# Kernel tuning notes

Hardware: AMD Instinct MI355X
Metric: run time of the kernel (lower is better)

Reference implementation:

```python
import jax, jax.numpy as jnp
import numpy as np

EPS = 1e-3


def setup_inputs() -> dict:
    key = jax.random.key(0)
    kq, kk, kv, kp = jax.random.split(key, 4)
    B, H, L, d = 4, 8, 8192, 64
    num_rows = int(d * np.log(d))  # 266, as in PerformerProjection
    q = jax.random.normal(kq, (B, H, L, d), dtype=jnp.float32)
    k = jax.random.normal(kk, (B, H, L, d), dtype=jnp.float32)
    v = jax.random.normal(kv, (B, H, L, d), dtype=jnp.float32)
    # Orthogonal-block projection matrix [num_rows, d] via QR (matches buffer init)
    rng = np.random.default_rng(0)
    blocks = []
    rows_left = num_rows
    while rows_left > 0:
        m = rng.standard_normal((d, d)).astype(np.float32)
        qm, _ = np.linalg.qr(m)
        blocks.append(qm.T[: min(d, rows_left)])
        rows_left -= d
    proj = jnp.asarray(np.concatenate(blocks, axis=0))  # [num_rows, d]
    return {"q": q, "k": k, "v": v, "proj": proj}


def reference(q, k, v, proj):
    # generalized_kernel: x @ proj.T, ReLU, + eps  -> features [B,H,L,R]
    qp = jax.nn.relu(jnp.einsum("bhld,rd->bhlr", q, proj)) + EPS
    kp = jax.nn.relu(jnp.einsum("bhld,rd->bhlr", k, proj)) + EPS
    # linear attention: D^{-1} (Q' ((K')^T V))
    k_sum = kp.sum(axis=-2)                       # [B,H,R]
    d_inv = 1.0 / jnp.einsum("bhlr,bhr->bhl", qp, k_sum)  # [B,H,L]
    kv = jnp.einsum("bhlr,bhld->bhrd", kp, v)     # [B,H,R,d]
    out = jnp.einsum("bhlr,bhrd->bhld", qp, kv)   # [B,H,L,d]
    return out * d_inv[..., None]
```

## Files before the change

### kernel.cpp

```cpp
#include <hip/hip_runtime.h>

typedef __attribute__((ext_vector_type(8))) short short8;
typedef __attribute__((ext_vector_type(4))) float f32x4;

#define MFMA16(a,b,c) __builtin_amdgcn_mfma_f32_16x16x32_bf16((a),(b),(c),0,0,0)

constexpr int BHC = 32;
constexpr int LEN = 8192;
constexpr int DD  = 64;
constexpr int RR  = 266;
constexpr int RP  = 272;
constexpr float EPSF = 1e-3f;

__device__ __forceinline__ unsigned short f2bf(float x) {
  unsigned u = __builtin_bit_cast(unsigned, x);
  return (unsigned short)((u + 0x7FFFu + ((u >> 16) & 1u)) >> 16);
}
__device__ __forceinline__ float bf2f(unsigned short h) {
  return __builtin_bit_cast(float, (unsigned)h << 16);
}
__device__ __forceinline__ void split2(float x, unsigned short& h, unsigned short& l) {
  h = f2bf(x);
  l = f2bf(x - bf2f(h));
}

__global__ __launch_bounds__(512, 1) void perf_kv_kernel(
    const float* __restrict__ kin, const float* __restrict__ vin,
    const float* __restrict__ proj,
    float* __restrict__ kv_ws, float* __restrict__ ksum_ws)
{
  __shared__ unsigned short K_hi[32*72], K_lo[32*72];
  __shared__ float V_lds[32*68];
  __shared__ unsigned int fT_hi[RP*20], fT_lo[RP*20];

  const int t = threadIdx.x;
  const int wid = t >> 6, lane = t & 63, g = lane >> 4, ln = lane & 15;
  const int bh = blockIdx.y;
  const float* kb = kin + (size_t)bh * LEN * DD + (size_t)blockIdx.x * 1024 * DD;
  const float* vb = vin + (size_t)bh * LEN * DD + (size_t)blockIdx.x * 1024 * DD;

  const int nrt1 = (wid == 7) ? 3 : 2;
  short8 Ph[3][2], Pl[3][2];
#pragma unroll
  for (int j = 0; j < 3; ++j) {
    const int rt = (j == 2) ? 16 : 2 * wid + j;
#pragma unroll
    for (int c = 0; c < 2; ++c) {
      const int r = rt * 16 + ln;
      float pv[8];
      if (j < nrt1 && r < RR) {
        const float4 a = *(const float4*)&proj[r * DD + c * 32 + g * 8];
        const float4 b = *(const float4*)&proj[r * DD + c * 32 + g * 8 + 4];
        pv[0]=a.x; pv[1]=a.y; pv[2]=a.z; pv[3]=a.w;
        pv[4]=b.x; pv[5]=b.y; pv[6]=b.z; pv[7]=b.w;
      } else {
#pragma unroll
        for (int i = 0; i < 8; ++i) pv[i] = 0.f;
      }
#pragma unroll
      for (int i = 0; i < 8; ++i) {
        unsigned short h, l; split2(pv[i], h, l);
        Ph[j][c][i] = (short)h; Pl[j][c][i] = (short)l;
      }
    }
  }

  f32x4 kvacc[9];
#pragma unroll
  for (int j = 0; j < 9; ++j) kvacc[j] = (f32x4){0.f,0.f,0.f,0.f};
  float ksacc[3] = {0.f, 0.f, 0.f};

  const int dt = wid & 3;
  const int rbase2 = (wid >> 2) * 9;
  const int nrt2 = (wid >> 2) ? 8 : 9;

  for (int s = 0; s < 32; ++s) {
    {
      const int l = t >> 4, c4 = t & 15;
      const float4 kv4 = *(const float4*)&kb[(size_t)(s*32 + l) * DD + c4*4];
      const float4 vv4 = *(const float4*)&vb[(size_t)(s*32 + l) * DD + c4*4];
      unsigned short h0,q0,h1,q1,h2,q2,h3,q3;
      split2(kv4.x,h0,q0); split2(kv4.y,h1,q1); split2(kv4.z,h2,q2); split2(kv4.w,h3,q3);
      *(ushort4*)&K_hi[l*72 + c4*4] = make_ushort4(h0,h1,h2,h3);
      *(ushort4*)&K_lo[l*72 + c4*4] = make_ushort4(q0,q1,q2,q3);
      *(float4*)&V_lds[l*68 + c4*4] = vv4;
    }
    __syncthreads();

    short8 KAh[2][2], KAl[2][2];
#pragma unroll
    for (int lt = 0; lt < 2; ++lt)
#pragma unroll
    for (int c = 0; c < 2; ++c) {
      KAh[lt][c] = *(const short8*)&K_hi[(lt*16+ln)*72 + c*32 + g*8];
      KAl[lt][c] = *(const short8*)&K_lo[(lt*16+ln)*72 + c*32 + g*8];
    }
#pragma unroll
    for (int j = 0; j < 3; ++j) if (j < nrt1) {
      const int rt = (j == 2) ? 16 : 2*wid + j;
      const int r = rt*16 + ln;
      const bool rok = r < RR;
#pragma unroll
      for (int lt = 0; lt < 2; ++lt) {
        f32x4 acc = {0.f,0.f,0.f,0.f};
#pragma unroll
        for (int c = 0; c < 2; ++c) {
          acc = MFMA16(KAh[lt][c], Ph[j][c], acc);
          acc = MFMA16(KAh[lt][c], Pl[j][c], acc);
          acc = MFMA16(KAl[lt][c], Ph[j][c], acc);
        }
        unsigned short h[4], q[4];
        float sum = 0.f;
#pragma unroll
        for (int reg = 0; reg < 4; ++reg) {
          const float fv = rok ? (fmaxf(acc[reg], 0.f) + EPSF) : 0.f;
          sum += fv;
          split2(fv, h[reg], q[reg]);
        }
        ksacc[j] += sum;
        *(uint2*)&fT_hi[r*20 + lt*8 + g*2] =
            make_uint2((unsigned)h[0] | ((unsigned)h[1]<<16),
                       (unsigned)h[2] | ((unsigned)h[3]<<16));
        *(uint2*)&fT_lo[r*20 + lt*8 + g*2] =
            make_uint2((unsigned)q[0] | ((unsigned)q[1]<<16),
                       (unsigned)q[2] | ((unsigned)q[3]<<16));
      }
    }
    __syncthreads();

    short8 VAh, VAl;
#pragma unroll
    for (int i = 0; i < 8; ++i) {
      const float v = V_lds[(g*8 + i)*68 + dt*16 + ln];
      unsigned short h, l; split2(v, h, l);
      VAh[i] = (short)h; VAl[i] = (short)l;
    }
#pragma unroll
    for (int j = 0; j < 9; ++j) if (j < nrt2) {
      const int rt = rbase2 + j;
      const short8 Bh = *(const short8*)&fT_hi[(rt*16+ln)*20 + g*4];
      const short8 Bl = *(const short8*)&fT_lo[(rt*16+ln)*20 + g*4];
      f32x4 a = kvacc[j];
      a = MFMA16(VAh, Bh, a);
      a = MFMA16(VAh, Bl, a);
      a = MFMA16(VAl, Bh, a);
      kvacc[j] = a;
    }
    __syncthreads();
  }

  float* kvb = kv_ws + (size_t)bh * DD * RP;
#pragma unroll
  for (int j = 0; j < 9; ++j) if (j < nrt2) {
    const int rt = rbase2 + j;
#pragma unroll
    for (int reg = 0; reg < 4; ++reg)
      atomicAdd(&kvb[(dt*16 + g*4 + reg) * RP + rt*16 + ln], kvacc[j][reg]);
  }
#pragma unroll
  for (int j = 0; j < 3; ++j) if (j < nrt1) {
    const int rt = (j == 2) ? 16 : 2*wid + j;
    float v = ksacc[j];
    v += __shfl_xor(v, 16);
    v += __shfl_xor(v, 32);
    if (lane < 16) atomicAdd(&ksum_ws[bh * RP + rt*16 + lane], v);
  }
}

__global__ __launch_bounds__(512, 1) void perf_out_kernel(
    const float* __restrict__ qin, const float* __restrict__ proj,
    const float* __restrict__ kv_ws, const float* __restrict__ ksum_ws,
    float* __restrict__ out)
{
  __shared__ unsigned short P_hi[RP*72], P_lo[RP*72];
  __shared__ unsigned short feat_hi[32*296], feat_lo[32*296];
  __shared__ unsigned short Q_hi[32*72], Q_lo[32*72];
  __shared__ float ksum_lds[RP];
  __shared__ float den_l[32];

  const int t = threadIdx.x;
  const int wid = t >> 6, lane = t & 63, g = lane >> 4, ln = lane & 15;
  const int bh = blockIdx.y;
  const float* qb = qin + (size_t)bh * LEN * DD + (size_t)blockIdx.x * 1024 * DD;
  float* ob = out + (size_t)bh * LEN * DD + (size_t)blockIdx.x * 1024 * DD;

  for (int idx = t; idx < RP * 16; idx += 512) {
    const int row = idx >> 4, c4 = idx & 15;
    float4 val = make_float4(0.f, 0.f, 0.f, 0.f);
    if (row < RR) val = *(const float4*)&proj[row * DD + c4 * 4];
    unsigned short h0,q0,h1,q1,h2,q2,h3,q3;
    split2(val.x,h0,q0); split2(val.y,h1,q1); split2(val.z,h2,q2); split2(val.w,h3,q3);
    *(ushort4*)&P_hi[row*72 + c4*4] = make_ushort4(h0,h1,h2,h3);
    *(ushort4*)&P_lo[row*72 + c4*4] = make_ushort4(q0,q1,q2,q3);
  }
  for (int idx = t; idx < 32 * 32; idx += 512) {
    const int row = idx >> 5, c = 272 + (idx & 31);
    if (c < 296) { feat_hi[row*296 + c] = 0; feat_lo[row*296 + c] = 0; }
  }
  if (t < RP) ksum_lds[t] = ksum_ws[bh*RP + t];

  const int dt = wid & 3;
  short8 KVh[9], KVl[9];
  {
    const float* kvr = kv_ws + ((size_t)bh*DD + dt*16 + ln) * RP;
#pragma unroll
    for (int kc = 0; kc < 9; ++kc) {
      const int r0 = kc*32 + g*8;
      float pv[8];
      if (r0 + 7 < RP) {
        const float4 a = *(const float4*)&kvr[r0];
        const float4 b = *(const float4*)&kvr[r0 + 4];
        pv[0]=a.x; pv[1]=a.y; pv[2]=a.z; pv[3]=a.w;
        pv[4]=b.x; pv[5]=b.y; pv[6]=b.z; pv[7]=b.w;
      } else {
#pragma unroll
        for (int i = 0; i < 8; ++i) pv[i] = 0.f;
      }
#pragma unroll
      for (int i = 0; i < 8; ++i) {
        unsigned short h, l; split2(pv[i], h, l);
        KVh[kc][i] = (short)h; KVl[kc][i] = (short)l;
      }
    }
  }

  const int nrt1 = (wid >= 6) ? 3 : 2;
  const int lt4 = wid >> 2, dt4 = wid & 3;

  __syncthreads();

  for (int s = 0; s < 32; ++s) {
    {
      const int l = t >> 4, c4 = t & 15;
      const float4 qv4 = *(const float4*)&qb[(size_t)(s*32 + l) * DD + c4*4];
      unsigned short h0,q0,h1,q1,h2,q2,h3,q3;
      split2(qv4.x,h0,q0); split2(qv4.y,h1,q1); split2(qv4.z,h2,q2); split2(qv4.w,h3,q3);
      *(ushort4*)&Q_hi[l*72 + c4*4] = make_ushort4(h0,h1,h2,h3);
      *(ushort4*)&Q_lo[l*72 + c4*4] = make_ushort4(q0,q1,q2,q3);
      if (t < 32) den_l[t] = 0.f;
    }
    __syncthreads();

#pragma unroll
    for (int j = 0; j < 3; ++j) if (j < nrt1) {
      const int rt = (j == 2) ? 16 : 2*wid + j;
      short8 PAh[2], PAl[2];
#pragma unroll
      for (int c = 0; c < 2; ++c) {
        PAh[c] = *(const short8*)&P_hi[(rt*16+ln)*72 + c*32 + g*8];
        PAl[c] = *(const short8*)&P_lo[(rt*16+ln)*72 + c*32 + g*8];
      }
#pragma unroll
      for (int lt = 0; lt < 2; ++lt) {
        if (j == 2 && lt != (wid & 1)) continue;
        f32x4 acc = {0.f,0.f,0.f,0.f};
#pragma unroll
        for (int c = 0; c < 2; ++c) {
          const short8 QBh = *(const short8*)&Q_hi[(lt*16+ln)*72 + c*32 + g*8];
          const short8 QBl = *(const short8*)&Q_lo[(lt*16+ln)*72 + c*32 + g*8];
          acc = MFMA16(PAh[c], QBh, acc);
          acc = MFMA16(PAh[c], QBl, acc);
          acc = MFMA16(PAl[c], QBh, acc);
        }
        unsigned short h[4], q[4];
        float dacc = 0.f;
#pragma unroll
        for (int reg = 0; reg < 4; ++reg) {
          const int r = rt*16 + g*4 + reg;
          const float fv = (r < RR) ? (fmaxf(acc[reg], 0.f) + EPSF) : 0.f;
          dacc += fv * ksum_lds[r];
          split2(fv, h[reg], q[reg]);
        }
        atomicAdd(&den_l[lt*16 + ln], dacc);
        *(ushort4*)&feat_hi[(lt*16+ln)*296 + rt*16 + g*4] = make_ushort4(h[0],h[1],h[2],h[3]);
        *(ushort4*)&feat_lo[(lt*16+ln)*296 + rt*16 + g*4] = make_ushort4(q[0],q[1],q[2],q[3]);
      }
    }
    __syncthreads();

    f32x4 oacc = {0.f,0.f,0.f,0.f};
#pragma unroll
    for (int kc = 0; kc < 9; ++kc) {
      const short8 Ah = *(const short8*)&feat_hi[(lt4*16+ln)*296 + kc*32 + g*8];
      const short8 Al = *(const short8*)&feat_lo[(lt4*16+ln)*296 + kc*32 + g*8];
      oacc = MFMA16(Ah, KVh[kc], oacc);
      oacc = MFMA16(Ah, KVl[kc], oacc);
      oacc = MFMA16(Al, KVh[kc], oacc);
    }
#pragma unroll
    for (int reg = 0; reg < 4; ++reg) {
      const int l = lt4*16 + g*4 + reg;
      ob[(size_t)(s*32 + l) * DD + dt4*16 + ln] = oacc[reg] / den_l[l];
    }
    __syncthreads();
  }
}

extern "C" void kernel_launch(void* const* d_in, const int* in_sizes, int n_in,
                              void* d_out, int out_size, void* d_ws, size_t ws_size,
                              hipStream_t stream) {
  (void)in_sizes; (void)n_in; (void)out_size; (void)ws_size;
  const float* q    = (const float*)d_in[0];
  const float* k    = (const float*)d_in[1];
  const float* v    = (const float*)d_in[2];
  const float* proj = (const float*)d_in[3];
  float* out     = (float*)d_out;
  float* kv_ws   = (float*)d_ws;
  float* ksum_ws = kv_ws + (size_t)BHC * DD * RP;

  size_t zbytes = ((size_t)BHC * DD * RP + (size_t)BHC * RP) * sizeof(float);
  hipMemsetAsync(d_ws, 0, zbytes, stream);

  perf_kv_kernel<<<dim3(8, BHC), dim3(512), 0, stream>>>(k, v, proj, kv_ws, ksum_ws);
  perf_out_kernel<<<dim3(8, BHC), dim3(512), 0, stream>>>(q, proj, kv_ws, ksum_ws, out);
}
```

Before: 450.6 us.

## Double grid size, reload projection per tile, and trim barriers in both kernels

Both kernels now process 512 rows per block instead of 1024, doubling the grid to 16x32 blocks so more CUs are busy. Projection fragments are no longer held in registers or an LDS copy; they are reloaded from global memory (L1/L2-cached) per tile, which frees registers and LDS. V is read straight from global instead of being staged through LDS. The next K/Q tile is loaded after the mid-iteration barrier, removing one sync per iteration, and den_l is double-buffered. MFMA accumulation is split into three independent chains to shorten dependency latency, at the cost of extra proj loads and twice as many atomic flushes to the workspace.

```diff
diff --git a/kernel.cpp b/kernel.cpp
--- a/kernel.cpp
+++ b/kernel.cpp
@@ -30,113 +30,107 @@
     float* __restrict__ kv_ws, float* __restrict__ ksum_ws)
 {
   __shared__ unsigned short K_hi[32*72], K_lo[32*72];
-  __shared__ float V_lds[32*68];
   __shared__ unsigned int fT_hi[RP*20], fT_lo[RP*20];
 
   const int t = threadIdx.x;
   const int wid = t >> 6, lane = t & 63, g = lane >> 4, ln = lane & 15;
   const int bh = blockIdx.y;
-  const float* kb = kin + (size_t)bh * LEN * DD + (size_t)blockIdx.x * 1024 * DD;
-  const float* vb = vin + (size_t)bh * LEN * DD + (size_t)blockIdx.x * 1024 * DD;
+  const float* kb = kin + (size_t)bh*LEN*DD + (size_t)blockIdx.x*512*DD;
+  const float* vb = vin + (size_t)bh*LEN*DD + (size_t)blockIdx.x*512*DD;
 
   const int nrt1 = (wid == 7) ? 3 : 2;
-  short8 Ph[3][2], Pl[3][2];
-#pragma unroll
-  for (int j = 0; j < 3; ++j) {
-    const int rt = (j == 2) ? 16 : 2 * wid + j;
-#pragma unroll
-    for (int c = 0; c < 2; ++c) {
-      const int r = rt * 16 + ln;
-      float pv[8];
-      if (j < nrt1 && r < RR) {
-        const float4 a = *(const float4*)&proj[r * DD + c * 32 + g * 8];
-        const float4 b = *(const float4*)&proj[r * DD + c * 32 + g * 8 + 4];
-        pv[0]=a.x; pv[1]=a.y; pv[2]=a.z; pv[3]=a.w;
-        pv[4]=b.x; pv[5]=b.y; pv[6]=b.z; pv[7]=b.w;
-      } else {
-#pragma unroll
-        for (int i = 0; i < 8; ++i) pv[i] = 0.f;
-      }
-#pragma unroll
-      for (int i = 0; i < 8; ++i) {
-        unsigned short h, l; split2(pv[i], h, l);
-        Ph[j][c][i] = (short)h; Pl[j][c][i] = (short)l;
-      }
-    }
-  }
+  const int dt = wid & 3, rbase2 = (wid >> 2) * 9, nrt2 = (wid >> 2) ? 8 : 9;
 
   f32x4 kvacc[9];
 #pragma unroll
   for (int j = 0; j < 9; ++j) kvacc[j] = (f32x4){0.f,0.f,0.f,0.f};
-  float ksacc[3] = {0.f, 0.f, 0.f};
-
-  const int dt = wid & 3;
-  const int rbase2 = (wid >> 2) * 9;
-  const int nrt2 = (wid >> 2) ? 8 : 9;
-
-  for (int s = 0; s < 32; ++s) {
-    {
-      const int l = t >> 4, c4 = t & 15;
-      const float4 kv4 = *(const float4*)&kb[(size_t)(s*32 + l) * DD + c4*4];
-      const float4 vv4 = *(const float4*)&vb[(size_t)(s*32 + l) * DD + c4*4];
-      unsigned short h0,q0,h1,q1,h2,q2,h3,q3;
-      split2(kv4.x,h0,q0); split2(kv4.y,h1,q1); split2(kv4.z,h2,q2); split2(kv4.w,h3,q3);
-      *(ushort4*)&K_hi[l*72 + c4*4] = make_ushort4(h0,h1,h2,h3);
-      *(ushort4*)&K_lo[l*72 + c4*4] = make_ushort4(q0,q1,q2,q3);
-      *(float4*)&V_lds[l*68 + c4*4] = vv4;
-    }
-    __syncthreads();
-
-    short8 KAh[2][2], KAl[2][2];
-#pragma unroll
-    for (int lt = 0; lt < 2; ++lt)
-#pragma unroll
-    for (int c = 0; c < 2; ++c) {
-      KAh[lt][c] = *(const short8*)&K_hi[(lt*16+ln)*72 + c*32 + g*8];
-      KAl[lt][c] = *(const short8*)&K_lo[(lt*16+ln)*72 + c*32 + g*8];
-    }
-#pragma unroll
-    for (int j = 0; j < 3; ++j) if (j < nrt1) {
-      const int rt = (j == 2) ? 16 : 2*wid + j;
-      const int r = rt*16 + ln;
-      const bool rok = r < RR;
-#pragma unroll
-      for (int lt = 0; lt < 2; ++lt) {
-        f32x4 acc = {0.f,0.f,0.f,0.f};
+  float ksacc[3] = {0.f,0.f,0.f};
+
+  const int sl = t >> 4, sc = t & 15;
+  {
+    const float4 k4 = *(const float4*)&kb[(size_t)sl*DD + sc*4];
+    unsigned short h0,q0,h1,q1,h2,q2,h3,q3;
+    split2(k4.x,h0,q0); split2(k4.y,h1,q1); split2(k4.z,h2,q2); split2(k4.w,h3,q3);
+    *(ushort4*)&K_hi[sl*72 + sc*4] = make_ushort4(h0,h1,h2,h3);
+    *(ushort4*)&K_lo[sl*72 + sc*4] = make_ushort4(q0,q1,q2,q3);
+  }
+  __syncthreads();
+
+  for (int s = 0; s < 16; ++s) {
+#pragma unroll
+    for (int lt = 0; lt < 2; ++lt) {
+      short8 KAh[2], KAl[2];
+#pragma unroll
+      for (int c = 0; c < 2; ++c) {
+        KAh[c] = *(const short8*)&K_hi[(lt*16+ln)*72 + c*32 + g*8];
+        KAl[c] = *(const short8*)&K_lo[(lt*16+ln)*72 + c*32 + g*8];
+      }
+#pragma unroll
+      for (int j = 0; j < 3; ++j) {
+        if (j >= nrt1) break;
+        const int rt = (j == 2) ? 16 : 2*wid + j;
+        const int r = rt*16 + ln;
+        const bool rok = r < RR;
+        short8 PBh[2], PBl[2];
 #pragma unroll
         for (int c = 0; c < 2; ++c) {
-          acc = MFMA16(KAh[lt][c], Ph[j][c], acc);
-          acc = MFMA16(KAh[lt][c], Pl[j][c], acc);
-          acc = MFMA16(KAl[lt][c], Ph[j][c], acc);
+          float pv[8];
+          if (rok) {
+            const float4 a = *(const float4*)&proj[r*DD + c*32 + g*8];
+            const float4 b = *(const float4*)&proj[r*DD + c*32 + g*8 + 4];
+            pv[0]=a.x; pv[1]=a.y; pv[2]=a.z; pv[3]=a.w;
+            pv[4]=b.x; pv[5]=b.y; pv[6]=b.z; pv[7]=b.w;
+          } else {
+#pragma unroll
+            for (int i2 = 0; i2 < 8; ++i2) pv[i2] = 0.f;
+          }
+#pragma unroll
+          for (int i2 = 0; i2 < 8; ++i2) {
+            unsigned short h, l2; split2(pv[i2], h, l2);
+            PBh[c][i2] = (short)h; PBl[c][i2] = (short)l2;
+          }
+        }
+        f32x4 a0 = {0.f,0.f,0.f,0.f}, a1 = a0, a2 = a0;
+#pragma unroll
+        for (int c = 0; c < 2; ++c) {
+          a0 = MFMA16(KAh[c], PBh[c], a0);
+          a1 = MFMA16(KAh[c], PBl[c], a1);
+          a2 = MFMA16(KAl[c], PBh[c], a2);
         }
         unsigned short h[4], q[4];
         float sum = 0.f;
 #pragma unroll
         for (int reg = 0; reg < 4; ++reg) {
-          const float fv = rok ? (fmaxf(acc[reg], 0.f) + EPSF) : 0.f;
+          const float fv = rok ? (fmaxf(a0[reg]+a1[reg]+a2[reg], 0.f) + EPSF) : 0.f;
           sum += fv;
           split2(fv, h[reg], q[reg]);
         }
         ksacc[j] += sum;
         *(uint2*)&fT_hi[r*20 + lt*8 + g*2] =
-            make_uint2((unsigned)h[0] | ((unsigned)h[1]<<16),
-                       (unsigned)h[2] | ((unsigned)h[3]<<16));
+            make_uint2((unsigned)h[0]|((unsigned)h[1]<<16), (unsigned)h[2]|((unsigned)h[3]<<16));
         *(uint2*)&fT_lo[r*20 + lt*8 + g*2] =
-            make_uint2((unsigned)q[0] | ((unsigned)q[1]<<16),
-                       (unsigned)q[2] | ((unsigned)q[3]<<16));
+            make_uint2((unsigned)q[0]|((unsigned)q[1]<<16), (unsigned)q[2]|((unsigned)q[3]<<16));
       }
     }
     __syncthreads();
 
+    if (s < 15) {
+      const float4 k4 = *(const float4*)&kb[(size_t)((s+1)*32 + sl)*DD + sc*4];
+      unsigned short h0,q0,h1,q1,h2,q2,h3,q3;
+      split2(k4.x,h0,q0); split2(k4.y,h1,q1); split2(k4.z,h2,q2); split2(k4.w,h3,q3);
+      *(ushort4*)&K_hi[sl*72 + sc*4] = make_ushort4(h0,h1,h2,h3);
+      *(ushort4*)&K_lo[sl*72 + sc*4] = make_ushort4(q0,q1,q2,q3);
+    }
     short8 VAh, VAl;
 #pragma unroll
     for (int i = 0; i < 8; ++i) {
-      const float v = V_lds[(g*8 + i)*68 + dt*16 + ln];
-      unsigned short h, l; split2(v, h, l);
-      VAh[i] = (short)h; VAl[i] = (short)l;
-    }
-#pragma unroll
-    for (int j = 0; j < 9; ++j) if (j < nrt2) {
+      const float v = vb[(size_t)(s*32 + g*8 + i)*DD + dt*16 + ln];
+      unsigned short h, l2; split2(v, h, l2);
+      VAh[i] = (short)h; VAl[i] = (short)l2;
+    }
+#pragma unroll
+    for (int j = 0; j < 9; ++j) {
+      if (j >= nrt2) break;
       const int rt = rbase2 + j;
       const short8 Bh = *(const short8*)&fT_hi[(rt*16+ln)*20 + g*4];
       const short8 Bl = *(const short8*)&fT_lo[(rt*16+ln)*20 + g*4];
@@ -151,19 +145,21 @@
 
   float* kvb = kv_ws + (size_t)bh * DD * RP;
 #pragma unroll
-  for (int j = 0; j < 9; ++j) if (j < nrt2) {
+  for (int j = 0; j < 9; ++j) {
+    if (j >= nrt2) break;
     const int rt = rbase2 + j;
 #pragma unroll
     for (int reg = 0; reg < 4; ++reg)
-      atomicAdd(&kvb[(dt*16 + g*4 + reg) * RP + rt*16 + ln], kvacc[j][reg]);
-  }
-#pragma unroll
-  for (int j = 0; j < 3; ++j) if (j < nrt1) {
+      atomicAdd(&kvb[(dt*16 + g*4 + reg)*RP + rt*16 + ln], kvacc[j][reg]);
+  }
+#pragma unroll
+  for (int j = 0; j < 3; ++j) {
+    if (j >= nrt1) break;
     const int rt = (j == 2) ? 16 : 2*wid + j;
     float v = ksacc[j];
     v += __shfl_xor(v, 16);
     v += __shfl_xor(v, 32);
-    if (lane < 16) atomicAdd(&ksum_ws[bh * RP + rt*16 + lane], v);
+    if (lane < 16) atomicAdd(&ksum_ws[bh*RP + rt*16 + lane], v);
   }
 }
 
@@ -172,37 +168,37 @@
     const float* __restrict__ kv_ws, const float* __restrict__ ksum_ws,
     float* __restrict__ out)
 {
-  __shared__ unsigned short P_hi[RP*72], P_lo[RP*72];
+  __shared__ unsigned short Q_hi[32*72], Q_lo[32*72];
   __shared__ unsigned short feat_hi[32*296], feat_lo[32*296];
-  __shared__ unsigned short Q_hi[32*72], Q_lo[32*72];
   __shared__ float ksum_lds[RP];
-  __shared__ float den_l[32];
+  __shared__ float den_l[2][32];
 
   const int t = threadIdx.x;
   const int wid = t >> 6, lane = t & 63, g = lane >> 4, ln = lane & 15;
   const int bh = blockIdx.y;
-  const float* qb = qin + (size_t)bh * LEN * DD + (size_t)blockIdx.x * 1024 * DD;
-  float* ob = out + (size_t)bh * LEN * DD + (size_t)blockIdx.x * 1024 * DD;
-
-  for (int idx = t; idx < RP * 16; idx += 512) {
-    const int row = idx >> 4, c4 = idx & 15;
-    float4 val = make_float4(0.f, 0.f, 0.f, 0.f);
-    if (row < RR) val = *(const float4*)&proj[row * DD + c4 * 4];
+  const float* qb = qin + (size_t)bh*LEN*DD + (size_t)blockIdx.x*512*DD;
+  float* outb = out + (size_t)bh*LEN*DD + (size_t)blockIdx.x*512*DD;
+
+  for (int idx = t; idx < 32*24; idx += 512) {
+    const int row = idx / 24, c = 272 + idx % 24;
+    feat_hi[row*296 + c] = 0; feat_lo[row*296 + c] = 0;
+  }
+  if (t < RP) ksum_lds[t] = ksum_ws[bh*RP + t];
+  if (t < 32) den_l[0][t] = 0.f;
+
+  const int sl = t >> 4, sc = t & 15;
+  {
+    const float4 q4 = *(const float4*)&qb[(size_t)sl*DD + sc*4];
     unsigned short h0,q0,h1,q1,h2,q2,h3,q3;
-    split2(val.x,h0,q0); split2(val.y,h1,q1); split2(val.z,h2,q2); split2(val.w,h3,q3);
-    *(ushort4*)&P_hi[row*72 + c4*4] = make_ushort4(h0,h1,h2,h3);
-    *(ushort4*)&P_lo[row*72 + c4*4] = make_ushort4(q0,q1,q2,q3);
-  }
-  for (int idx = t; idx < 32 * 32; idx += 512) {
-    const int row = idx >> 5, c = 272 + (idx & 31);
-    if (c < 296) { feat_hi[row*296 + c] = 0; feat_lo[row*296 + c] = 0; }
-  }
-  if (t < RP) ksum_lds[t] = ksum_ws[bh*RP + t];
-
-  const int dt = wid & 3;
+    split2(q4.x,h0,q0); split2(q4.y,h1,q1); split2(q4.z,h2,q2); split2(q4.w,h3,q3);
+    *(ushort4*)&Q_hi[sl*72 + sc*4] = make_ushort4(h0,h1,h2,h3);
+    *(ushort4*)&Q_lo[sl*72 + sc*4] = make_ushort4(q0,q1,q2,q3);
+  }
+
+  const int lt4 = wid >> 2, dt4 = wid & 3;
   short8 KVh[9], KVl[9];
   {
-    const float* kvr = kv_ws + ((size_t)bh*DD + dt*16 + ln) * RP;
+    const float* kvr = kv_ws + ((size_t)bh*DD + dt4*16 + ln) * RP;
 #pragma unroll
     for (int kc = 0; kc < 9; ++kc) {
       const int r0 = kc*32 + g*8;
@@ -218,79 +214,95 @@
       }
 #pragma unroll
       for (int i = 0; i < 8; ++i) {
-        unsigned short h, l; split2(pv[i], h, l);
-        KVh[kc][i] = (short)h; KVl[kc][i] = (short)l;
+        unsigned short h, l2; split2(pv[i], h, l2);
+        KVh[kc][i] = (short)h; KVl[kc][i] = (short)l2;
       }
     }
   }
 
   const int nrt1 = (wid >= 6) ? 3 : 2;
-  const int lt4 = wid >> 2, dt4 = wid & 3;
-
   __syncthreads();
 
-  for (int s = 0; s < 32; ++s) {
-    {
-      const int l = t >> 4, c4 = t & 15;
-      const float4 qv4 = *(const float4*)&qb[(size_t)(s*32 + l) * DD + c4*4];
-      unsigned short h0,q0,h1,q1,h2,q2,h3,q3;
-      split2(qv4.x,h0,q0); split2(qv4.y,h1,q1); split2(qv4.z,h2,q2); split2(qv4.w,h3,q3);
-      *(ushort4*)&Q_hi[l*72 + c4*4] = make_ushort4(h0,h1,h2,h3);
-      *(ushort4*)&Q_lo[l*72 + c4*4] = make_ushort4(q0,q1,q2,q3);
-      if (t < 32) den_l[t] = 0.f;
-    }
-    __syncthreads();
-
-#pragma unroll
-    for (int j = 0; j < 3; ++j) if (j < nrt1) {
-      const int rt = (j == 2) ? 16 : 2*wid + j;
-      short8 PAh[2], PAl[2];
+  for (int s = 0; s < 16; ++s) {
+#pragma unroll
+    for (int lt = 0; lt < 2; ++lt) {
+      short8 QBh[2], QBl[2];
 #pragma unroll
       for (int c = 0; c < 2; ++c) {
-        PAh[c] = *(const short8*)&P_hi[(rt*16+ln)*72 + c*32 + g*8];
-        PAl[c] = *(const short8*)&P_lo[(rt*16+ln)*72 + c*32 + g*8];
-      }
-#pragma unroll
-      for (int lt = 0; lt < 2; ++lt) {
+        QBh[c] = *(const short8*)&Q_hi[(lt*16+ln)*72 + c*32 + g*8];
+        QBl[c] = *(const short8*)&Q_lo[(lt*16+ln)*72 + c*32 + g*8];
+      }
+#pragma unroll
+      for (int j = 0; j < 3; ++j) {
+        if (j >= nrt1) break;
         if (j == 2 && lt != (wid & 1)) continue;
-        f32x4 acc = {0.f,0.f,0.f,0.f};
+        const int rt = (j == 2) ? 16 : 2*wid + j;
+        const int ra = rt*16 + ln;
+        const bool raok = ra < RR;
+        short8 PAh[2], PAl[2];
 #pragma unroll
         for (int c = 0; c < 2; ++c) {
-          const short8 QBh = *(const short8*)&Q_hi[(lt*16+ln)*72 + c*32 + g*8];
-          const short8 QBl = *(const short8*)&Q_lo[(lt*16+ln)*72 + c*32 + g*8];
-          acc = MFMA16(PAh[c], QBh, acc);
-          acc = MFMA16(PAh[c], QBl, acc);
-          acc = MFMA16(PAl[c], QBh, acc);
+          float pv[8];
+          if (raok) {
+            const float4 a = *(const float4*)&proj[ra*DD + c*32 + g*8];
+            const float4 b = *(const float4*)&proj[ra*DD + c*32 + g*8 + 4];
+            pv[0]=a.x; pv[1]=a.y; pv[2]=a.z; pv[3]=a.w;
+            pv[4]=b.x; pv[5]=b.y; pv[6]=b.z; pv[7]=b.w;
+          } else {
+#pragma unroll
+            for (int i2 = 0; i2 < 8; ++i2) pv[i2] = 0.f;
+          }
+#pragma unroll
+          for (int i2 = 0; i2 < 8; ++i2) {
+            unsigned short h, l2; split2(pv[i2], h, l2);
+            PAh[c][i2] = (short)h; PAl[c][i2] = (short)l2;
+          }
+        }
+        f32x4 a0 = {0.f,0.f,0.f,0.f}, a1 = a0, a2 = a0;
+#pragma unroll
+        for (int c = 0; c < 2; ++c) {
+          a0 = MFMA16(PAh[c], QBh[c], a0);
+          a1 = MFMA16(PAh[c], QBl[c], a1);
+          a2 = MFMA16(PAl[c], QBh[c], a2);
         }
         unsigned short h[4], q[4];
         float dacc = 0.f;
 #pragma unroll
         for (int reg = 0; reg < 4; ++reg) {
-          const int r = rt*16 + g*4 + reg;
-          const float fv = (r < RR) ? (fmaxf(acc[reg], 0.f) + EPSF) : 0.f;
-          dacc += fv * ksum_lds[r];
+          const int rr = rt*16 + g*4 + reg;
+          const float fv = (rr < RR) ? (fmaxf(a0[reg]+a1[reg]+a2[reg], 0.f) + EPSF) : 0.f;
+          dacc += fv * ksum_lds[rr];
           split2(fv, h[reg], q[reg]);
         }
-        atomicAdd(&den_l[lt*16 + ln], dacc);
+        atomicAdd(&den_l[s & 1][lt*16 + ln], dacc);
         *(ushort4*)&feat_hi[(lt*16+ln)*296 + rt*16 + g*4] = make_ushort4(h[0],h[1],h[2],h[3]);
         *(ushort4*)&feat_lo[(lt*16+ln)*296 + rt*16 + g*4] = make_ushort4(q[0],q[1],q[2],q[3]);
       }
     }
     __syncthreads();
 
-    f32x4 oacc = {0.f,0.f,0.f,0.f};
+    if (s < 15) {
+      const float4 q4 = *(const float4*)&qb[(size_t)((s+1)*32 + sl)*DD + sc*4];
+      unsigned short h0,q0,h1,q1,h2,q2,h3,q3;
+      split2(q4.x,h0,q0); split2(q4.y,h1,q1); split2(q4.z,h2,q2); split2(q4.w,h3,q3);
+      *(ushort4*)&Q_hi[sl*72 + sc*4] = make_ushort4(h0,h1,h2,h3);
+      *(ushort4*)&Q_lo[sl*72 + sc*4] = make_ushort4(q0,q1,q2,q3);
+    }
+    if (t < 32) den_l[(s+1) & 1][t] = 0.f;
+    f32x4 oacc0 = {0.f,0.f,0.f,0.f}, oacc1 = oacc0, oacc2 = oacc0;
 #pragma unroll
     for (int kc = 0; kc < 9; ++kc) {
       const short8 Ah = *(const short8*)&feat_hi[(lt4*16+ln)*296 + kc*32 + g*8];
       const short8 Al = *(const short8*)&feat_lo[(lt4*16+ln)*296 + kc*32 + g*8];
-      oacc = MFMA16(Ah, KVh[kc], oacc);
-      oacc = MFMA16(Ah, KVl[kc], oacc);
-      oacc = MFMA16(Al, KVh[kc], oacc);
+      oacc0 = MFMA16(Ah, KVh[kc], oacc0);
+      oacc1 = MFMA16(Ah, KVl[kc], oacc1);
+      oacc2 = MFMA16(Al, KVh[kc], oacc2);
     }
 #pragma unroll
     for (int reg = 0; reg < 4; ++reg) {
       const int l = lt4*16 + g*4 + reg;
-      ob[(size_t)(s*32 + l) * DD + dt4*16 + ln] = oacc[reg] / den_l[l];
+      const float o = oacc0[reg] + oacc1[reg] + oacc2[reg];
+      outb[(size_t)(s*32 + l)*DD + dt4*16 + ln] = o / den_l[s & 1][l];
     }
     __syncthreads();
   }
@@ -311,6 +323,6 @@
   size_t zbytes = ((size_t)BHC * DD * RP + (size_t)BHC * RP) * sizeof(float);
   hipMemsetAsync(d_ws, 0, zbytes, stream);
 
-  perf_kv_kernel<<<dim3(8, BHC), dim3(512), 0, stream>>>(k, v, proj, kv_ws, ksum_ws);
-  perf_out_kernel<<<dim3(8, BHC), dim3(512), 0, stream>>>(q, proj, kv_ws, ksum_ws, out);
-}
+  perf_kv_kernel<<<dim3(16, BHC), dim3(512), 0, stream>>>(k, v, proj, kv_ws, ksum_ws);
+  perf_out_kernel<<<dim3(16, BHC), dim3(512), 0, stream>>>(q, proj, kv_ws, ksum_ws, out);
+}
```

After: 681.8 us. 51.3% more time.
